# Kernel tuning notes

Measured on AMD Instinct MI355X. Metric: run time of the kernel, lower is better.

## Reference

```python
import jax, jax.numpy as jnp
import numpy as np

N = 50000   # nodes
E = 800000  # edges
G = 64      # graphs in batch
D = 128     # num_input
H = 128     # num_hidden
O = 10      # num_output


def _linear_params(key, fan_in, fan_out):
    k1, k2 = jax.random.split(key)
    s = 1.0 / np.sqrt(fan_in)
    W = jax.random.uniform(k1, (fan_out, fan_in), jnp.float32, -s, s)
    b = jax.random.uniform(k2, (fan_out,), jnp.float32, -s, s)
    return W, b


def setup_inputs() -> dict:
    key = jax.random.key(0)
    ks = jax.random.split(key, 12)
    x = jax.random.normal(ks[0], (N, D), jnp.float32)
    edge_index = jax.random.randint(ks[1], (2, E), 0, N, dtype=jnp.int32).astype(jnp.int64)
    batch = jnp.sort(jax.random.randint(ks[2], (N,), 0, G, dtype=jnp.int32)).astype(jnp.int64)

    W_rel1, b_rel1 = _linear_params(ks[3], D, H)
    W_root1, _ = _linear_params(ks[4], D, H)
    W_rel2, b_rel2 = _linear_params(ks[5], H, H)
    W_root2, _ = _linear_params(ks[6], H, H)
    W_rel3, b_rel3 = _linear_params(ks[7], H, H)
    W_root3, _ = _linear_params(ks[8], H, H)
    W1, b1 = _linear_params(ks[9], 2 * H, 128)
    W2, b2 = _linear_params(ks[10], 128, 64)
    W3, b3 = _linear_params(ks[11], 64, O)

    return dict(x=x, edge_index=edge_index, batch=batch,
                W_rel1=W_rel1, b_rel1=b_rel1, W_root1=W_root1,
                W_rel2=W_rel2, b_rel2=b_rel2, W_root2=W_root2,
                W_rel3=W_rel3, b_rel3=b_rel3, W_root3=W_root3,
                W1=W1, b1=b1, W2=W2, b2=b2, W3=W3, b3=b3)


def _graph_conv(x, src, dst, W_rel, b_rel, W_root):
    # PyG GraphConv (aggr='add'): out_i = W_rel @ sum_{j->i} x_j + b_rel + W_root @ x_i
    agg = jax.ops.segment_sum(x[src], dst, num_segments=N)  # [N, d]
    return agg @ W_rel.T + b_rel + x @ W_root.T


def _pool(x, batch):
    # concat(global_max_pool, global_mean_pool) -> [G, 2d]
    mx = jax.ops.segment_max(x, batch, num_segments=G)
    mx = jnp.where(jnp.isfinite(mx), mx, 0.0)  # guard empty segments
    sm = jax.ops.segment_sum(x, batch, num_segments=G)
    cnt = jax.ops.segment_sum(jnp.ones((x.shape[0], 1), x.dtype), batch, num_segments=G)
    mean = sm / jnp.maximum(cnt, 1.0)
    return jnp.concatenate([mx, mean], axis=1)


def reference(x, edge_index, batch,
              W_rel1, b_rel1, W_root1,
              W_rel2, b_rel2, W_root2,
              W_rel3, b_rel3, W_root3,
              W1, b1, W2, b2, W3, b3):
    src, dst = edge_index[0], edge_index[1]
    h = jax.nn.relu(_graph_conv(x, src, dst, W_rel1, b_rel1, W_root1))
    x1 = _pool(h, batch)
    h = jax.nn.relu(_graph_conv(h, src, dst, W_rel2, b_rel2, W_root2))
    x2 = _pool(h, batch)
    h = jax.nn.relu(_graph_conv(h, src, dst, W_rel3, b_rel3, W_root3))
    x3 = _pool(h, batch)
    node_embs = h
    graph_emb = x1 + x2 + x3           # [G, 2H]
    z = jax.nn.relu(graph_emb @ W1.T + b1)
    z = jax.nn.relu(z @ W2.T + b2)     # dropout p=0 -> no-op
    logits = z @ W3.T + b3             # [G, O]
    return logits, node_embs, graph_emb
```

## Files before the change

kernel.cpp:

```cpp
#include <hip/hip_runtime.h>
#include <hip/hip_bf16.h>

#define NN 50000
#define EE 800000
#define GG 64
#define NBUCK 196
#define ABLOCKS 125
#define CHUNK 6400
#define BCAP 8192
#define SPANCAP 512

typedef __attribute__((ext_vector_type(8))) short bf16x8;
typedef __attribute__((ext_vector_type(4))) float f32x4;

__device__ __forceinline__ float bflo(unsigned u) { return __uint_as_float(u << 16); }
__device__ __forceinline__ float bfhi(unsigned u) { return __uint_as_float(u & 0xffff0000u); }
__device__ __forceinline__ float b2f(unsigned short s) { return __uint_as_float(((unsigned)s) << 16); }
__device__ __forceinline__ unsigned short f2bf(float f) {
    __hip_bfloat16 h = __float2bfloat16(f);
    union { __hip_bfloat16 h; unsigned short u; } cv; cv.h = h; return cv.u;
}

__global__ void detect_kernel(const unsigned* __restrict__ xw,
                              const unsigned* __restrict__ eiw,
                              int* __restrict__ flags) {
    __shared__ int s_cnt, s_nz;
    if (threadIdx.x == 0) { s_cnt = 0; s_nz = 0; }
    __syncthreads();
    int cnt = 0;
    for (int i = threadIdx.x; i < 4096; i += 256) {
        unsigned w = xw[(size_t)i * 711];
        unsigned elo = (w >> 7) & 0xFF;
        if (elo >= 100 && elo <= 140) cnt++;
    }
    int nz = 0;
    for (int i = threadIdx.x; i < 1024; i += 256) {
        unsigned w = eiw[(size_t)i * 1560 + 1];
        if (w != 0) nz++;
    }
    atomicAdd(&s_cnt, cnt);
    atomicAdd(&s_nz, nz);
    __syncthreads();
    if (threadIdx.x == 0) {
        flags[0] = (s_cnt < 3600) ? 1 : 0;
        flags[1] = (s_nz  < 8)    ? 1 : 0;
    }
}

struct WPtrs { const void* p[15]; };

__global__ __launch_bounds__(256) void prep_kernel(const void* __restrict__ xsrc,
                                                   const unsigned* __restrict__ eiw,
                                                   WPtrs wp,
                                                   unsigned short* __restrict__ arena,
                                                   int* __restrict__ counts,
                                                   uint4* __restrict__ zero_region,
                                                   const int* __restrict__ flags) {
    const int b = blockIdx.x;
    const int tid = threadIdx.x;
    const int isF32 = flags[0];

    if (b < 3125) {
        const int total4 = NN * 128 / 4;
        for (int i = b * 256 + tid; i < total4; i += 800000) {
            uint2 o;
            if (isF32) {
                float4 f = ((const float4*)xsrc)[i];
                o.x = (unsigned)f2bf(f.x) | ((unsigned)f2bf(f.y) << 16);
                o.y = (unsigned)f2bf(f.z) | ((unsigned)f2bf(f.w) << 16);
            } else {
                o = ((const uint2*)xsrc)[i];
            }
            ((uint2*)arena)[i] = o;
        }
    } else if (b < 3674) {
        const int cnt[15] = {16384,128,16384, 16384,128,16384, 16384,128,16384,
                             32768,128,8192,64,640,10};
        const int dst[15] = {19200000,19232768,19216384, 19232896,19265664,19249280,
                             19265792,19298560,19282176,
                             19298688,19331456,19331584,19339776,19339840,19340480};
        const int total = 140490;
        int i = (b - 3125) * 256 + tid;
        if (i < total) {
            int seg = 0, base = 0;
            while (i - base >= cnt[seg]) { base += cnt[seg]; ++seg; }
            int off = i - base;
            const void* s = wp.p[seg];
            arena[dst[seg] + off] =
                isF32 ? f2bf(((const float*)s)[off]) : ((const unsigned short*)s)[off];
        }
    } else if (b < 3799) {
        __shared__ int hist[256];
        hist[tid] = 0;
        __syncthreads();
        const int i64 = flags[1];
        const int e0 = (b - 3674) * CHUNK;
        for (int it = 0; it < CHUNK / 256; ++it) {
            int e = e0 + it * 256 + tid;
            int d = (int)(i64 ? eiw[(size_t)2 * (EE + e)] : eiw[EE + e]);
            atomicAdd(&hist[d >> 8], 1);
        }
        __syncthreads();
        counts[(b - 3674) * 256 + tid] = hist[tid];
    } else {
        zero_region[(b - 3799) * 256 + tid] = (uint4){0, 0, 0, 0};
    }
}

__global__ __launch_bounds__(256) void bucket_offsets(const int* __restrict__ counts,
                                                      int* __restrict__ offsets,
                                                      int* __restrict__ bucket_base) {
    __shared__ int s[256];
    const int t = threadIdx.x;
    int col = 0;
    for (int b = 0; b < ABLOCKS; ++b) col += counts[b * 256 + t];
    s[t] = col;
    __syncthreads();
    for (int d = 1; d < 256; d <<= 1) {
        int x = (t >= d) ? s[t - d] : 0;
        __syncthreads();
        s[t] += x;
        __syncthreads();
    }
    int base = s[t] - col;
    bucket_base[t] = base;
    if (t == 255) bucket_base[256] = s[255];
    int run = base;
    for (int b = 0; b < ABLOCKS; ++b) {
        offsets[b * 256 + t] = run;
        run += counts[b * 256 + t];
    }
}

__global__ __launch_bounds__(256) void bucket_scatter(const unsigned* __restrict__ eiw,
                                                      const int* __restrict__ offsets,
                                                      unsigned* __restrict__ packed,
                                                      const int* __restrict__ flags) {
    __shared__ int cur[256];
    cur[threadIdx.x] = offsets[blockIdx.x * 256 + threadIdx.x];
    __syncthreads();
    int i64 = flags[1];
    int e0 = blockIdx.x * CHUNK;
    for (int it = 0; it < CHUNK / 256; ++it) {
        int e = e0 + it * 256 + threadIdx.x;
        int s = (int)(i64 ? eiw[(size_t)2 * e]        : eiw[e]);
        int d = (int)(i64 ? eiw[(size_t)2 * (EE + e)] : eiw[EE + e]);
        int pos = atomicAdd(&cur[d >> 8], 1);
        packed[pos] = ((unsigned)s << 8) | (unsigned)(d & 255);
    }
}

__global__ __launch_bounds__(256) void bucket_sort(const unsigned* __restrict__ packed,
                                                   const int* __restrict__ bucket_base,
                                                   int* __restrict__ csr_src,
                                                   int* __restrict__ row_ptr) {
    __shared__ unsigned sbuf[BCAP];
    __shared__ int hist[256];
    __shared__ int cur[256];
    const int t = threadIdx.x;
    const int b = blockIdx.x;
    const int lo = bucket_base[b];
    int n = bucket_base[b + 1] - lo;
    if (n > BCAP) n = BCAP;

    hist[t] = 0;
    __syncthreads();
    for (int i = t; i < n; i += 256) {
        unsigned p = packed[lo + i];
        sbuf[i] = p;
        atomicAdd(&hist[p & 255], 1);
    }
    __syncthreads();
    int v = hist[t];
    __shared__ int s[256];
    s[t] = v;
    __syncthreads();
    for (int d = 1; d < 256; d <<= 1) {
        int x = (t >= d) ? s[t - d] : 0;
        __syncthreads();
        s[t] += x;
        __syncthreads();
    }
    int start = s[t] - v;
    int node = b * 256 + t;
    if (node < NN) row_ptr[node] = lo + start;
    if (b == 0 && t == 0) row_ptr[NN] = EE;
    cur[t] = start;
    __syncthreads();
    for (int i = t; i < n; i += 256) {
        unsigned p = sbuf[i];
        int pos = atomicAdd(&cur[p & 255], 1);
        csr_src[lo + pos] = (int)(p >> 8);
    }
}

__global__ __launch_bounds__(256, 8) void conv_fused(const unsigned short* __restrict__ hin,
                                                     const int* __restrict__ row_ptr,
                                                     const int* __restrict__ csr_src,
                                                     const unsigned short* __restrict__ Wrel,
                                                     const unsigned short* __restrict__ Wroot,
                                                     const unsigned short* __restrict__ brel,
                                                     const unsigned* __restrict__ bw,
                                                     unsigned* __restrict__ pmx,
                                                     float* __restrict__ psum,
                                                     unsigned short* __restrict__ outb,
                                                     void* __restrict__ outG,
                                                     const int* __restrict__ flags) {
    __shared__ __align__(16) unsigned short tile[16][136];
    __shared__ int sbatch[16];
    __shared__ int s_rp[17];
    __shared__ int s_idx[SPANCAP];

    const int tid  = threadIdx.x;
    const int wv   = tid >> 6;
    const int lane = tid & 63;
    const int m0   = blockIdx.x * 16;

    if (tid < 17) s_rp[tid] = row_ptr[m0 + tid];
    if (tid >= 32 && tid < 48) {
        const int i64 = flags[1];
        int rr = m0 + (tid - 32);
        sbatch[tid - 32] = (int)(i64 ? bw[(size_t)2 * rr] : bw[rr]);
    }
    __syncthreads();
    const int base = s_rp[0];
    const int span = s_rp[16] - base;
    const int nst  = (span < SPANCAP) ? span : SPANCAP;
    for (int i = tid; i < nst; i += 256) s_idx[i] = csr_src[base + i];
    __syncthreads();

    const int qd  = lane >> 4;
    const int l16 = lane & 15;
    const int lr  = wv * 4 + qd;
    const int jb  = s_rp[lr]     - base;
    const int je  = s_rp[lr + 1] - base;
    const uint4* h16 = (const uint4*)hin;

    float a0 = 0.f, a1 = 0.f, a2 = 0.f, a3 = 0.f,
          a4 = 0.f, a5 = 0.f, a6 = 0.f, a7 = 0.f;

    if (span <= SPANCAP) {
        int j = jb;
        for (; j + 8 <= je; j += 8) {
            int idx[8];
            #pragma unroll
            for (int q = 0; q < 8; ++q) idx[q] = s_idx[j + q];
            uint4 u[8];
            #pragma unroll
            for (int q = 0; q < 8; ++q) u[q] = h16[(size_t)idx[q] * 16 + l16];
            #pragma unroll
            for (int q = 0; q < 8; ++q) {
                a0 += bflo(u[q].x); a1 += bfhi(u[q].x);
                a2 += bflo(u[q].y); a3 += bfhi(u[q].y);
                a4 += bflo(u[q].z); a5 += bfhi(u[q].z);
                a6 += bflo(u[q].w); a7 += bfhi(u[q].w);
            }
        }
        if (j < je) {
            #pragma unroll
            for (int q = 0; q < 8; ++q) {
                int ii = j + q;
                int ic = (ii < je - 1) ? ii : (je - 1);
                float sc = (ii < je) ? 1.f : 0.f;
                uint4 u = h16[(size_t)s_idx[ic] * 16 + l16];
                a0 = fmaf(bflo(u.x), sc, a0); a1 = fmaf(bfhi(u.x), sc, a1);
                a2 = fmaf(bflo(u.y), sc, a2); a3 = fmaf(bfhi(u.y), sc, a3);
                a4 = fmaf(bflo(u.z), sc, a4); a5 = fmaf(bfhi(u.z), sc, a5);
                a6 = fmaf(bflo(u.w), sc, a6); a7 = fmaf(bfhi(u.w), sc, a7);
            }
        }
    } else {
        for (int j = jb; j < je; j += 8) {
            #pragma unroll
            for (int q = 0; q < 8; ++q) {
                int ii = j + q;
                int ic = (ii < je - 1) ? ii : (je - 1);
                float sc = (ii < je) ? 1.f : 0.f;
                uint4 u = h16[(size_t)csr_src[base + ic] * 16 + l16];
                a0 = fmaf(bflo(u.x), sc, a0); a1 = fmaf(bfhi(u.x), sc, a1);
                a2 = fmaf(bflo(u.y), sc, a2); a3 = fmaf(bfhi(u.y), sc, a3);
                a4 = fmaf(bflo(u.z), sc, a4); a5 = fmaf(bfhi(u.z), sc, a5);
                a6 = fmaf(bflo(u.w), sc, a6); a7 = fmaf(bfhi(u.w), sc, a7);
            }
        }
    }

    {
        uint4 o;
        o.x = (unsigned)f2bf(a0) | ((unsigned)f2bf(a1) << 16);
        o.y = (unsigned)f2bf(a2) | ((unsigned)f2bf(a3) << 16);
        o.z = (unsigned)f2bf(a4) | ((unsigned)f2bf(a5) << 16);
        o.w = (unsigned)f2bf(a6) | ((unsigned)f2bf(a7) << 16);
        *(uint4*)&tile[lr][l16 * 8] = o;
    }
    __syncthreads();

    const int mrow = lane & 15;
    const int quad = lane >> 4;
    const int r    = m0 + mrow;

    f32x4 acc[2];
    acc[0] = (f32x4){0.f, 0.f, 0.f, 0.f};
    acc[1] = (f32x4){0.f, 0.f, 0.f, 0.f};

    #pragma unroll
    for (int kk = 0; kk < 8; ++kk) {
        const unsigned short* Bs = (kk < 4) ? Wrel : Wroot;
        const int kc = (kk & 3) * 32 + quad * 8;
        bf16x8 a;
        if (kk < 4) a = *(const bf16x8*)&tile[mrow][kc];
        else        a = *(const bf16x8*)(hin + (size_t)r * 128 + kc);
        #pragma unroll
        for (int n = 0; n < 2; ++n) {
            const int col0 = (wv * 2 + n) * 16;
            bf16x8 b = *(const bf16x8*)(Bs + (size_t)(col0 + mrow) * 128 + kc);
            acc[n] = __builtin_amdgcn_mfma_f32_16x16x32_bf16(a, b, acc[n], 0, 0, 0);
        }
    }

    __syncthreads();

    #pragma unroll
    for (int n = 0; n < 2; ++n) {
        const int col = (wv * 2 + n) * 16 + mrow;
        const float bias = b2f(brel[col]);
        #pragma unroll
        for (int i = 0; i < 4; ++i) {
            const int lrow = quad * 4 + i;
            float v = fmaxf(acc[n][i] + bias, 0.f);
            tile[lrow][col] = f2bf(v);
        }
    }
    __syncthreads();

    const int isF32 = flags[0];
    {
        const int lr2 = tid >> 4;
        const int c16 = tid & 15;
        uint4 v = *(const uint4*)&tile[lr2][c16 * 8];
        ((uint4*)outb)[(size_t)(m0 + lr2) * 16 + c16] = v;
        if (outG) {
            if (isF32) {
                float4* p = (float4*)outG + 160 + (size_t)(m0 + lr2) * 32 + c16 * 2;
                p[0] = (float4){bflo(v.x), bfhi(v.x), bflo(v.y), bfhi(v.y)};
                p[1] = (float4){bflo(v.z), bfhi(v.z), bflo(v.w), bfhi(v.w)};
            } else {
                uint4* p = (uint4*)((unsigned short*)outG + 640);
                p[(size_t)(m0 + lr2) * 16 + c16] = v;
            }
        }
    }

    if (tid < 128) {
        const int col = tid;
        const int slice = blockIdx.x & 7;
        int curg = sbatch[0];
        float mx = 0.f, sm = 0.f;
        for (int rr = 0; rr < 16; ++rr) {
            int g = sbatch[rr];
            if (g != curg) {
                atomicMax(&pmx[(slice * GG + curg) * 128 + col], __float_as_uint(mx));
                unsafeAtomicAdd(&psum[(slice * GG + curg) * 128 + col], sm);
                curg = g; mx = 0.f; sm = 0.f;
            }
            float v = b2f(tile[rr][col]);
            mx = fmaxf(mx, v);
            sm += v;
        }
        atomicMax(&pmx[(slice * GG + curg) * 128 + col], __float_as_uint(mx));
        unsafeAtomicAdd(&psum[(slice * GG + curg) * 128 + col], sm);
    }
}

__global__ __launch_bounds__(256) void mlp_kernel(const unsigned* __restrict__ pmxL,
                                                  const float* __restrict__ psum,
                                                  const unsigned* __restrict__ bw,
                                                  const unsigned short* __restrict__ W1,
                                                  const unsigned short* __restrict__ b1,
                                                  const unsigned short* __restrict__ W2,
                                                  const unsigned short* __restrict__ b2,
                                                  const unsigned short* __restrict__ W3,
                                                  const unsigned short* __restrict__ b3,
                                                  void* __restrict__ out,
                                                  const int* __restrict__ flags) {
    int g = blockIdx.x;
    int t = threadIdx.x;
    int isF32 = flags[0];
    int i64 = flags[1];
    __shared__ float sge[256];
    __shared__ float sz1[128];
    __shared__ float sz2[64];

    int lo = 0, hi = NN;
    while (lo < hi) {
        int mid = (lo + hi) >> 1;
        int bv = (int)(i64 ? bw[(size_t)2 * mid] : bw[mid]);
        if (bv < g) lo = mid + 1; else hi = mid;
    }
    int start = lo;
    hi = NN;
    while (lo < hi) {
        int mid = (lo + hi) >> 1;
        int bv = (int)(i64 ? bw[(size_t)2 * mid] : bw[mid]);
        if (bv < g + 1) lo = mid + 1; else hi = mid;
    }
    int cnt = lo - start;

    float v;
    if (t < 128) {
        v = 0.f;
        #pragma unroll
        for (int L = 0; L < 3; ++L) {
            float m = 0.f;
            #pragma unroll
            for (int s = 0; s < 8; ++s)
                m = fmaxf(m, __uint_as_float(pmxL[((L * 8 + s) * GG + g) * 128 + t]));
            v += m;
        }
    } else {
        float sm = 0.f;
        #pragma unroll
        for (int s = 0; s < 8; ++s) sm += psum[(s * GG + g) * 128 + (t - 128)];
        v = sm / fmaxf((float)cnt, 1.f);
    }
    sge[t] = v;
    size_t geo = (size_t)640 + (size_t)NN * 128 + (size_t)g * 256 + t;
    if (isF32) ((float*)out)[geo] = v;
    else       ((unsigned short*)out)[geo] = f2bf(v);
    __syncthreads();

    if (t < 128) {
        float acc = b2f(b1[t]);
        for (int k = 0; k < 256; ++k) acc = fmaf(sge[k], b2f(W1[t * 256 + k]), acc);
        sz1[t] = fmaxf(acc, 0.f);
    }
    __syncthreads();
    if (t < 64) {
        float acc = b2f(b2[t]);
        for (int k = 0; k < 128; ++k) acc = fmaf(sz1[k], b2f(W2[t * 128 + k]), acc);
        sz2[t] = fmaxf(acc, 0.f);
    }
    __syncthreads();
    if (t < 10) {
        float acc = b2f(b3[t]);
        for (int k = 0; k < 64; ++k) acc = fmaf(sz2[k], b2f(W3[t * 64 + k]), acc);
        size_t o = (size_t)g * 10 + t;
        if (isF32) ((float*)out)[o] = acc;
        else       ((unsigned short*)out)[o] = f2bf(acc);
    }
}

#define XBF_OFF   0
#define HA_OFF    6400000
#define HB_OFF    12800000
#define WR1_OFF   19200000
#define WO1_OFF   19216384
#define BR1_OFF   19232768
#define WR2_OFF   19232896
#define WO2_OFF   19249280
#define BR2_OFF   19265664
#define WR3_OFF   19265792
#define WO3_OFF   19282176
#define BR3_OFF   19298560
#define W1_OFF    19298688
#define B1_OFF    19331456
#define W2_OFF    19331584
#define B2_OFF    19339776
#define W3_OFF    19339840
#define B3_OFF    19340480
#define ARENA_END 19340490

extern "C" void kernel_launch(void* const* d_in, const int* in_sizes, int n_in,
                              void* d_out, int out_size, void* d_ws, size_t ws_size,
                              hipStream_t stream) {
    unsigned short* arena = (unsigned short*)d_ws;
    size_t intBase = ((size_t)ARENA_END * 2 + 255) & ~(size_t)255;
    char* ib = (char*)d_ws + intBase;
    int*      row_ptr = (int*)ib;
    int*      csr_src = (int*)(ib + 200064);
    unsigned* packed  = (unsigned*)(ib + 3400064);
    int*      counts  = (int*)(ib + 6600064);
    int*      offsets = (int*)(ib + 6728064);
    int*      bbase   = (int*)(ib + 6856064);
    unsigned* pmxL    = (unsigned*)(ib + 6857344);
    float*    psum    = (float*)(ib + 7643776);
    int*      flags   = (int*)(ib + 7905920);

    const unsigned* eiw = (const unsigned*)d_in[1];
    const unsigned* bw  = (const unsigned*)d_in[2];
    dim3 blk(256);

    detect_kernel<<<1, 256, 0, stream>>>((const unsigned*)d_in[0], eiw, flags);

    WPtrs wp;
    for (int i = 0; i < 15; ++i) wp.p[i] = d_in[3 + i];
    prep_kernel<<<4055, blk, 0, stream>>>(d_in[0], eiw, wp, arena, counts,
                                          (uint4*)pmxL, flags);

    bucket_offsets<<<1, blk, 0, stream>>>(counts, offsets, bbase);
    bucket_scatter<<<ABLOCKS, blk, 0, stream>>>(eiw, offsets, packed, flags);
    bucket_sort<<<NBUCK, blk, 0, stream>>>(packed, bbase, csr_src, row_ptr);

    const int convGrid = NN / 16;

    conv_fused<<<convGrid, blk, 0, stream>>>(arena + XBF_OFF, row_ptr, csr_src,
                                             arena + WR1_OFF, arena + WO1_OFF, arena + BR1_OFF,
                                             bw, pmxL, psum, arena + HA_OFF, nullptr, flags);
    conv_fused<<<convGrid, blk, 0, stream>>>(arena + HA_OFF, row_ptr, csr_src,
                                             arena + WR2_OFF, arena + WO2_OFF, arena + BR2_OFF,
                                             bw, pmxL + 65536, psum, arena + HB_OFF, nullptr, flags);
    conv_fused<<<convGrid, blk, 0, stream>>>(arena + HB_OFF, row_ptr, csr_src,
                                             arena + WR3_OFF, arena + WO3_OFF, arena + BR3_OFF,
                                             bw, pmxL + 131072, psum, arena + XBF_OFF, d_out, flags);

    mlp_kernel<<<GG, blk, 0, stream>>>(pmxL, psum, bw,
                                       arena + W1_OFF, arena + B1_OFF,
                                       arena + W2_OFF, arena + B2_OFF,
                                       arena + W3_OFF, arena + B3_OFF, d_out, flags);
}
```

Measured before the change: 343.2 us.

## Write per-block pool partials to buffer instead of atomics, reduce in MLP kernel

Each conv block now stores the max and sum of its leading run of same-graph rows into a per-block partial buffer with plain stores. Only rows belonging to a different graph than row 0 still go through the global atomicMax and atomicAdd. The MLP kernel then loops over the blocks that lie wholly inside each graph and reduces those partials. This is meant to remove atomic contention on the pooling slices, at the cost of extra workspace, about 800 extra serial reads per thread in the 64-block MLP kernel, and a fallback path when the workspace is too small.

```diff
diff --git a/kernel.cpp b/kernel.cpp
--- a/kernel.cpp
+++ b/kernel.cpp
@@ -9,6 +9,8 @@
 #define CHUNK 6400
 #define BCAP 8192
 #define SPANCAP 512
+#define PARTN 3125
+#define PSZ 400000
 
 typedef __attribute__((ext_vector_type(8))) short bf16x8;
 typedef __attribute__((ext_vector_type(4))) float f32x4;
@@ -203,6 +205,7 @@
                                                      const unsigned* __restrict__ bw,
                                                      unsigned* __restrict__ pmx,
                                                      float* __restrict__ psum,
+                                                     float* __restrict__ ppart,
                                                      unsigned short* __restrict__ outb,
                                                      void* __restrict__ outG,
                                                      const int* __restrict__ flags) {
@@ -354,26 +357,40 @@
     if (tid < 128) {
         const int col = tid;
         const int slice = blockIdx.x & 7;
-        int curg = sbatch[0];
+        int rr = 0;
         float mx = 0.f, sm = 0.f;
-        for (int rr = 0; rr < 16; ++rr) {
-            int g = sbatch[rr];
-            if (g != curg) {
-                atomicMax(&pmx[(slice * GG + curg) * 128 + col], __float_as_uint(mx));
-                unsafeAtomicAdd(&psum[(slice * GG + curg) * 128 + col], sm);
-                curg = g; mx = 0.f; sm = 0.f;
-            }
-            float v = b2f(tile[rr][col]);
-            mx = fmaxf(mx, v);
-            sm += v;
-        }
-        atomicMax(&pmx[(slice * GG + curg) * 128 + col], __float_as_uint(mx));
-        unsafeAtomicAdd(&psum[(slice * GG + curg) * 128 + col], sm);
+        if (ppart) {
+            const int g0 = sbatch[0];
+            for (; rr < 16 && sbatch[rr] == g0; ++rr) {
+                float v = b2f(tile[rr][col]);
+                mx = fmaxf(mx, v); sm += v;
+            }
+            ppart[(size_t)blockIdx.x * 128 + col] = mx;
+            ppart[(size_t)PSZ + (size_t)blockIdx.x * 128 + col] = sm;
+            mx = 0.f; sm = 0.f;
+        }
+        if (rr < 16) {
+            int curg = sbatch[rr];
+            for (; rr < 16; ++rr) {
+                int g = sbatch[rr];
+                if (g != curg) {
+                    atomicMax(&pmx[(slice * GG + curg) * 128 + col], __float_as_uint(mx));
+                    unsafeAtomicAdd(&psum[(slice * GG + curg) * 128 + col], sm);
+                    curg = g; mx = 0.f; sm = 0.f;
+                }
+                float v = b2f(tile[rr][col]);
+                mx = fmaxf(mx, v);
+                sm += v;
+            }
+            atomicMax(&pmx[(slice * GG + curg) * 128 + col], __float_as_uint(mx));
+            unsafeAtomicAdd(&psum[(slice * GG + curg) * 128 + col], sm);
+        }
     }
 }
 
 __global__ __launch_bounds__(256) void mlp_kernel(const unsigned* __restrict__ pmxL,
                                                   const float* __restrict__ psum,
+                                                  const float* __restrict__ part,
                                                   const unsigned* __restrict__ bw,
                                                   const unsigned short* __restrict__ W1,
                                                   const unsigned short* __restrict__ b1,
@@ -406,6 +423,9 @@
     }
     int cnt = lo - start;
 
+    int b_lo = (start + 15) >> 4;
+    int b_hi = (cnt > 0) ? ((start + cnt - 1) >> 4) : (b_lo - 1);
+
     float v;
     if (t < 128) {
         v = 0.f;
@@ -415,12 +435,25 @@
             #pragma unroll
             for (int s = 0; s < 8; ++s)
                 m = fmaxf(m, __uint_as_float(pmxL[((L * 8 + s) * GG + g) * 128 + t]));
+            if (part) {
+                const float* pm = part + (size_t)L * 2 * PSZ;
+                for (int b = b_lo; b <= b_hi; ++b)
+                    m = fmaxf(m, pm[(size_t)b * 128 + t]);
+            }
             v += m;
         }
     } else {
         float sm = 0.f;
         #pragma unroll
         for (int s = 0; s < 8; ++s) sm += psum[(s * GG + g) * 128 + (t - 128)];
+        if (part) {
+            #pragma unroll
+            for (int L = 0; L < 3; ++L) {
+                const float* ps = part + (size_t)L * 2 * PSZ + PSZ;
+                for (int b = b_lo; b <= b_hi; ++b)
+                    sm += ps[(size_t)b * 128 + (t - 128)];
+            }
+        }
         v = sm / fmaxf((float)cnt, 1.f);
     }
     sge[t] = v;
@@ -485,6 +518,10 @@
     unsigned* pmxL    = (unsigned*)(ib + 6857344);
     float*    psum    = (float*)(ib + 7643776);
     int*      flags   = (int*)(ib + 7905920);
+    float*    part    = (float*)(ib + 7906048);
+
+    size_t need = intBase + 7906048 + (size_t)3 * 2 * PSZ * 4;
+    float* partP = (ws_size >= need) ? part : nullptr;
 
     const unsigned* eiw = (const unsigned*)d_in[1];
     const unsigned* bw  = (const unsigned*)d_in[2];
@@ -505,15 +542,21 @@
 
     conv_fused<<<convGrid, blk, 0, stream>>>(arena + XBF_OFF, row_ptr, csr_src,
                                              arena + WR1_OFF, arena + WO1_OFF, arena + BR1_OFF,
-                                             bw, pmxL, psum, arena + HA_OFF, nullptr, flags);
+                                             bw, pmxL, psum,
+                                             partP ? partP : nullptr,
+                                             arena + HA_OFF, nullptr, flags);
     conv_fused<<<convGrid, blk, 0, stream>>>(arena + HA_OFF, row_ptr, csr_src,
                                              arena + WR2_OFF, arena + WO2_OFF, arena + BR2_OFF,
-                                             bw, pmxL + 65536, psum, arena + HB_OFF, nullptr, flags);
+                                             bw, pmxL + 65536, psum,
+                                             partP ? partP + (size_t)2 * PSZ : nullptr,
+                                             arena + HB_OFF, nullptr, flags);
     conv_fused<<<convGrid, blk, 0, stream>>>(arena + HB_OFF, row_ptr, csr_src,
                                              arena + WR3_OFF, arena + WO3_OFF, arena + BR3_OFF,
-                                             bw, pmxL + 131072, psum, arena + XBF_OFF, d_out, flags);
-
-    mlp_kernel<<<GG, blk, 0, stream>>>(pmxL, psum, bw,
+                                             bw, pmxL + 131072, psum,
+                                             partP ? partP + (size_t)4 * PSZ : nullptr,
+                                             arena + XBF_OFF, d_out, flags);
+
+    mlp_kernel<<<GG, blk, 0, stream>>>(pmxL, psum, partP, bw,
                                        arena + W1_OFF, arena + B1_OFF,
                                        arena + W2_OFF, arena + B2_OFF,
                                        arena + W3_OFF, arena + B3_OFF, d_out, flags);
```

Measured after the change: 380.5 us. 1.11x slower.
